# Performance work log

Measured on AMD Instinct MI355X. Metric: run time of the kernel, lower is better.

Reference implementation:

```python
import jax, jax.numpy as jnp
import numpy as np

B, L, D = 4, 4096, 1024
C = 8.0  # fixed exponent scale from the module (self.c = 8)


def setup_inputs() -> dict:
    key = jax.random.key(0)
    ks = jax.random.split(key, 4)
    std = 1.0 / np.sqrt(D)  # kaiming normal, fan_in, linear
    x = jax.random.normal(ks[0], (B, L, D), dtype=jnp.float32)
    Wa = jax.random.normal(ks[1], (D, D), dtype=jnp.float32) * std
    Wx = jax.random.normal(ks[2], (D, D), dtype=jnp.float32) * std
    ba = jnp.zeros((D,), dtype=jnp.float32)
    bx = jnp.zeros((D,), dtype=jnp.float32)
    # lmbd ~ U(0.9, 0.999)
    lmbd = 0.9 + 0.099 * jax.random.uniform(ks[3], (D,), dtype=jnp.float32)
    return {"x": x, "Wa": Wa, "Wx": Wx, "ba": ba, "bx": bx, "lmbd": lmbd}


def reference(x, Wa, Wx, ba, bx, lmbd):
    # a = sigmoid(lmbd) computed once at init in the original module
    log_a = jnp.log(jax.nn.sigmoid(lmbd))  # [D], negative
    # Batched projections upfront (F.linear uses W @ x^T, i.e. x @ W.T)
    r = jax.nn.sigmoid(jnp.einsum('bld,hd->blh', x, Wa) + ba)  # recurrence gate
    i = jax.nn.sigmoid(jnp.einsum('bld,hd->blh', x, Wx) + bx)  # input gate
    a_t = jnp.exp(C * r * log_a)                 # a ** (c * r), [B,L,D]
    b_t = jnp.sqrt(1.0 - a_t * a_t) * (i * x)    # [B,L,D]
    # Linear recurrence h_t = a_t * h_{t-1} + b_t, h_0 = 0
    def step(h, ab):
        at, bt = ab
        h = at * h + bt
        return h, h
    h0 = jnp.zeros((x.shape[0], x.shape[2]), dtype=x.dtype)
    _, y = jax.lax.scan(step, h0, (jnp.swapaxes(a_t, 0, 1), jnp.swapaxes(b_t, 0, 1)))
    return jnp.swapaxes(y, 0, 1)  # [B, L, D]
```

## Files before the change

kernel.cpp:

```cpp
#include <hip/hip_runtime.h>
#include <stdint.h>
#include <math.h>


#define D_DIM 1024
#define L_DIM 4096
#define B_DIM 4
#define M_DIM (B_DIM * L_DIM)
#define N_DIM (2 * D_DIM)
#define K_DIM D_DIM
#define NC 32
#define CL (L_DIM / NC)
#define L2E 1.4426950408889634f

typedef __attribute__((ext_vector_type(8))) short short8;
typedef __attribute__((ext_vector_type(4))) short short4v;
typedef __attribute__((ext_vector_type(4))) float float4v;

__device__ __forceinline__ unsigned short f2bf(float f) {
  unsigned u = __float_as_uint(f);
  u += 0x7fffu + ((u >> 16) & 1u);
  return (unsigned short)(u >> 16);
}
__device__ __forceinline__ float bf2f(unsigned short h) {
  return __uint_as_float((unsigned)h << 16);
}
__device__ __forceinline__ short f2h(float f) {
  _Float16 h = (_Float16)f;
  return __builtin_bit_cast(short, h);
}

#define NX16 (M_DIM * K_DIM / 8)
#define NW16 (N_DIM * K_DIM / 8)

__global__ void pack_all(const float* __restrict__ x, const float* __restrict__ Wa,
                         const float* __restrict__ Wx, short* __restrict__ Xs,
                         short* __restrict__ Ws) {
  int t = blockIdx.x * 256 + threadIdx.x;
  const float* src;
  short8* dst;
  int u;
  if (t < NX16) {
    u = t; src = x; dst = (short8*)Xs;
  } else {
    u = t - NX16;
    if (u >= NW16) return;
    dst = (short8*)Ws;
    int row = ((u >> 11) << 4) | (u & 15);
    src = (row < D_DIM) ? Wa : (Wx - (size_t)D_DIM * K_DIM);
  }
  int r  = u & 15;
  int kc = (u >> 4) & 3;
  int k0 = (u >> 6) & 31;
  int R  = u >> 11;
  int m = R * 16 + r;
  int k = (k0 * 4 + kc) * 8;
  const float4v* s4 = (const float4v*)(src + (size_t)m * 1024 + k);
  float4v v0 = s4[0], v1 = s4[1];
  short8 o;
  o[0] = (short)f2bf(v0.x); o[1] = (short)f2bf(v0.y);
  o[2] = (short)f2bf(v0.z); o[3] = (short)f2bf(v0.w);
  o[4] = (short)f2bf(v1.x); o[5] = (short)f2bf(v1.y);
  o[6] = (short)f2bf(v1.z); o[7] = (short)f2bf(v1.w);
  dst[u] = o;
}

__global__ __launch_bounds__(256, 4) void gemm_gates(
    const short* __restrict__ Xs,
    const short* __restrict__ Ws,
    const float* __restrict__ xf,
    const float* __restrict__ ba,
    const float* __restrict__ bx,
    const float* __restrict__ lmbd,
    short* __restrict__ e_out,
    unsigned short* __restrict__ g_out)
{
  __shared__ __align__(16) char smem[17664];

  const int tile_n = blockIdx.x * 128;
  const int tile_m = blockIdx.y * 128;
  const int tid  = threadIdx.x;
  const int wave = tid >> 6;
  const int lane = tid & 63;
  const int row16 = lane & 15;
  const int quad  = lane >> 4;
  const int wave_m = (wave & 1) * 64;
  const int wave_n = (wave >> 1) * 64;

  short* As = (short*)smem;
  short* Bs = (short*)(smem + 8192);
  char* AsB = smem;
  char* BsB = smem + 8192;

  float4v acc[4][4] = {};

  for (int kk = 0; kk < 32; ++kk) {
#pragma unroll
    for (int p = 0; p < 2; ++p) {
      const int G = p * 4 + wave;
      const size_t RgA = (size_t)((tile_m >> 4) + G);
      const size_t RgB = (size_t)((tile_n >> 4) + G);
      __builtin_amdgcn_global_load_lds(
          (const __attribute__((address_space(1))) void*)(Xs + ((RgA * 32 + kk) * 64 + lane) * 8),
          (__attribute__((address_space(3))) void*)(AsB + G * 1024),
          16, 0, 0);
      __builtin_amdgcn_global_load_lds(
          (const __attribute__((address_space(1))) void*)(Ws + ((RgB * 32 + kk) * 64 + lane) * 8),
          (__attribute__((address_space(3))) void*)(BsB + G * 1024),
          16, 0, 0);
    }
    __syncthreads();

    short8 af[4], bfr[4];
#pragma unroll
    for (int i = 0; i < 4; ++i)
      af[i] = *(const short8*)&As[((wave & 1) * 4 + i) * 512 + lane * 8];
#pragma unroll
    for (int i = 0; i < 4; ++i)
      bfr[i] = *(const short8*)&Bs[((wave >> 1) * 4 + i) * 512 + lane * 8];

#pragma unroll
    for (int mi = 0; mi < 4; ++mi)
#pragma unroll
      for (int ni = 0; ni < 4; ++ni)
        acc[mi][ni] = __builtin_amdgcn_mfma_f32_16x16x32_bf16(af[mi], bfr[ni], acc[mi][ni], 0, 0, 0);
    __syncthreads();
  }

  float* Ts = (float*)smem + (size_t)wave * (16 * 68);
  const int colg = (lane & 15) * 4;
  const int rrow = lane >> 4;
  const bool is_a = (tile_n < D_DIM);
  const int ch0 = (is_a ? tile_n : tile_n - D_DIM) + wave_n + colg;

  float4v bias4, la84;
  if (is_a) {
    bias4 = *(const float4v*)(ba + ch0);
    float4v lm4 = *(const float4v*)(lmbd + ch0);
#pragma unroll
    for (int k = 0; k < 4; ++k)
      la84[k] = -8.0f * __builtin_amdgcn_logf(1.0f + __builtin_amdgcn_exp2f(-lm4[k] * L2E));
  } else {
    bias4 = *(const float4v*)(bx + ch0);
  }

#pragma unroll
  for (int mi = 0; mi < 4; ++mi) {
#pragma unroll
    for (int ni = 0; ni < 4; ++ni)
#pragma unroll
      for (int r = 0; r < 4; ++r)
        Ts[(quad * 4 + r) * 68 + ni * 16 + row16] = acc[mi][ni][r];
#pragma unroll
    for (int j = 0; j < 4; ++j) {
      int lr = j * 4 + rrow;
      float4v z = *(const float4v*)&Ts[lr * 68 + colg];
      size_t gm = (size_t)(tile_m + wave_m + mi * 16 + lr);
      short4v o;
      if (is_a) {
#pragma unroll
        for (int k = 0; k < 4; ++k) {
          float s = __builtin_amdgcn_rcpf(1.0f + __builtin_amdgcn_exp2f(-(z[k] + bias4[k]) * L2E));
          o[k] = f2h(s * la84[k]);
        }
        *(short4v*)(e_out + gm * D_DIM + ch0) = o;
      } else {
        float4v xv = *(const float4v*)(xf + gm * D_DIM + ch0);
#pragma unroll
        for (int k = 0; k < 4; ++k) {
          float s = __builtin_amdgcn_rcpf(1.0f + __builtin_amdgcn_exp2f(-(z[k] + bias4[k]) * L2E));
          o[k] = (short)f2bf(s * xv[k]);
        }
        *(short4v*)((short*)g_out + gm * D_DIM + ch0) = o;
      }
    }
  }
}

__global__ void scan_phase1(const short* __restrict__ e, const unsigned short* __restrict__ g,
                            float* __restrict__ P, float* __restrict__ Q) {
  int d = blockIdx.x * 256 + threadIdx.x;
  int c = blockIdx.y;
  int b = blockIdx.z;
  const size_t base = ((size_t)(b * L_DIM + c * CL)) * D_DIM + d;
  float Pv = 1.0f, Qv = 0.0f;
#pragma unroll 4
  for (int t = 0; t < CL; ++t) {
    float ev = (float)__builtin_bit_cast(_Float16, e[base + (size_t)t * D_DIM]);
    float at = __builtin_amdgcn_exp2f(ev);
    float gv = bf2f(g[base + (size_t)t * D_DIM]);
    float bt = sqrtf(fmaxf(1.0f - at * at, 0.0f)) * gv;
    Qv = fmaf(at, Qv, bt);
    Pv *= at;
  }
  int idx = (b * NC + c) * D_DIM + d;
  P[idx] = Pv;
  Q[idx] = Qv;
}

__global__ void scan_phase3(const short* __restrict__ e, const unsigned short* __restrict__ g,
                            const float* __restrict__ P, const float* __restrict__ Q,
                            float* __restrict__ y) {
  int d = blockIdx.x * 256 + threadIdx.x;
  int c = blockIdx.y;
  int b = blockIdx.z;
  float h = 0.0f;
#pragma unroll 4
  for (int cc = 0; cc < c; ++cc) {
    int idx = (b * NC + cc) * D_DIM + d;
    h = fmaf(P[idx], h, Q[idx]);
  }
  const size_t base = ((size_t)(b * L_DIM + c * CL)) * D_DIM + d;
#pragma unroll 4
  for (int t = 0; t < CL; ++t) {
    float ev = (float)__builtin_bit_cast(_Float16, e[base + (size_t)t * D_DIM]);
    float at = __builtin_amdgcn_exp2f(ev);
    float gv = bf2f(g[base + (size_t)t * D_DIM]);
    float bt = sqrtf(fmaxf(1.0f - at * at, 0.0f)) * gv;
    h = fmaf(at, h, bt);
    y[base + (size_t)t * D_DIM] = h;
  }
}

extern "C" void kernel_launch(void* const* d_in, const int* in_sizes, int n_in,
                              void* d_out, int out_size, void* d_ws, size_t ws_size,
                              hipStream_t stream) {
  const float* x    = (const float*)d_in[0];
  const float* Wa   = (const float*)d_in[1];
  const float* Wx   = (const float*)d_in[2];
  const float* ba   = (const float*)d_in[3];
  const float* bx   = (const float*)d_in[4];
  const float* lmbd = (const float*)d_in[5];
  float* y = (float*)d_out;

  char* ws = (char*)d_ws;
  short* Xs             = (short*)ws;
  short* Wsz            = (short*)(ws + 33554432);
  short* e_buf          = (short*)(ws + 37748736);
  unsigned short* g_buf = (unsigned short*)(ws + 71303168);
  float* P              = (float*)(ws + 104857600);
  float* Q              = (float*)(ws + 105381888);

  pack_all<<<(NX16 + NW16) / 256, 256, 0, stream>>>(x, Wa, Wx, Xs, Wsz);

  dim3 gg(N_DIM / 128, M_DIM / 128);
  gemm_gates<<<gg, 256, 0, stream>>>(Xs, Wsz, x, ba, bx, lmbd, e_buf, g_buf);

  dim3 sg(D_DIM / 256, NC, B_DIM);
  scan_phase1<<<sg, 256, 0, stream>>>(e_buf, g_buf, P, Q);
  scan_phase3<<<sg, 256, 0, stream>>>(e_buf, g_buf, P, Q, y);
}
```

Baseline: 250.5 us.

## Fuse scan phases with decoupled look-back and read bf16 x in gate epilogue

Merges the two scan kernels into one. Each chunk computes its local (P,Q), waits on the previous chunk's published carry through a flag-tagged 64-bit slot, publishes its own carry, then runs the output pass. This removes one kernel launch and the O(NC) serial prefix over P/Q per chunk. The slots are zeroed inside the pack kernel. Separately, the gate epilogue reads x from the packed bf16 buffer instead of fp32, halving that read at a small precision cost. The spin-wait depends on earlier chunks being scheduled first, since the grid is ordered by chunk index, and it serializes the carry chain across 32 chunks.

```diff
diff --git a/kernel.cpp b/kernel.cpp
--- a/kernel.cpp
+++ b/kernel.cpp
@@ -32,22 +32,26 @@
 
 #define NX16 (M_DIM * K_DIM / 8)
 #define NW16 (N_DIM * K_DIM / 8)
+#define NSLOTS (B_DIM * NC * D_DIM)
 
 __global__ void pack_all(const float* __restrict__ x, const float* __restrict__ Wa,
                          const float* __restrict__ Wx, short* __restrict__ Xs,
-                         short* __restrict__ Ws) {
+                         short* __restrict__ Ws, unsigned long long* __restrict__ slots) {
   int t = blockIdx.x * 256 + threadIdx.x;
   const float* src;
   short8* dst;
   int u;
   if (t < NX16) {
     u = t; src = x; dst = (short8*)Xs;
-  } else {
+  } else if (t < NX16 + NW16) {
     u = t - NX16;
-    if (u >= NW16) return;
     dst = (short8*)Ws;
     int row = ((u >> 11) << 4) | (u & 15);
     src = (row < D_DIM) ? Wa : (Wx - (size_t)D_DIM * K_DIM);
+  } else {
+    int s = t - NX16 - NW16;
+    if (s < NSLOTS) slots[s] = 0ULL;
+    return;
   }
   int r  = u & 15;
   int kc = (u >> 4) & 3;
@@ -68,7 +72,6 @@
 __global__ __launch_bounds__(256, 4) void gemm_gates(
     const short* __restrict__ Xs,
     const short* __restrict__ Ws,
-    const float* __restrict__ xf,
     const float* __restrict__ ba,
     const float* __restrict__ bx,
     const float* __restrict__ lmbd,
@@ -143,6 +146,7 @@
   } else {
     bias4 = *(const float4v*)(bx + ch0);
   }
+  const size_t xs_ch = ((size_t)(ch0 >> 5) * 4 + ((ch0 >> 3) & 3)) * 16 * 8 + (ch0 & 7);
 
 #pragma unroll
   for (int mi = 0; mi < 4; ++mi) {
@@ -165,11 +169,11 @@
         }
         *(short4v*)(e_out + gm * D_DIM + ch0) = o;
       } else {
-        float4v xv = *(const float4v*)(xf + gm * D_DIM + ch0);
+        short4v xq = *(const short4v*)(Xs + ((gm >> 4) * 32 * 64 + (gm & 15)) * 8 + xs_ch);
 #pragma unroll
         for (int k = 0; k < 4; ++k) {
           float s = __builtin_amdgcn_rcpf(1.0f + __builtin_amdgcn_exp2f(-(z[k] + bias4[k]) * L2E));
-          o[k] = (short)f2bf(s * xv[k]);
+          o[k] = (short)f2bf(s * bf2f((unsigned short)xq[k]));
         }
         *(short4v*)((short*)g_out + gm * D_DIM + ch0) = o;
       }
@@ -177,12 +181,14 @@
   }
 }
 
-__global__ void scan_phase1(const short* __restrict__ e, const unsigned short* __restrict__ g,
-                            float* __restrict__ P, float* __restrict__ Q) {
+__global__ __launch_bounds__(256) void scan_fused(
+    const short* __restrict__ e, const unsigned short* __restrict__ g,
+    unsigned long long* __restrict__ slots, float* __restrict__ y) {
   int d = blockIdx.x * 256 + threadIdx.x;
   int c = blockIdx.y;
   int b = blockIdx.z;
   const size_t base = ((size_t)(b * L_DIM + c * CL)) * D_DIM + d;
+
   float Pv = 1.0f, Qv = 0.0f;
 #pragma unroll 4
   for (int t = 0; t < CL; ++t) {
@@ -193,24 +199,24 @@
     Qv = fmaf(at, Qv, bt);
     Pv *= at;
   }
-  int idx = (b * NC + c) * D_DIM + d;
-  P[idx] = Pv;
-  Q[idx] = Qv;
-}
-
-__global__ void scan_phase3(const short* __restrict__ e, const unsigned short* __restrict__ g,
-                            const float* __restrict__ P, const float* __restrict__ Q,
-                            float* __restrict__ y) {
-  int d = blockIdx.x * 256 + threadIdx.x;
-  int c = blockIdx.y;
-  int b = blockIdx.z;
-  float h = 0.0f;
-#pragma unroll 4
-  for (int cc = 0; cc < c; ++cc) {
-    int idx = (b * NC + cc) * D_DIM + d;
-    h = fmaf(P[idx], h, Q[idx]);
-  }
-  const size_t base = ((size_t)(b * L_DIM + c * CL)) * D_DIM + d;
+
+  float Hin = 0.0f;
+  if (c > 0) {
+    unsigned long long* sp = slots + ((size_t)(b * NC + c - 1) * D_DIM + d);
+    unsigned long long v = atomicAdd(sp, 0ULL);
+    while ((unsigned)(v >> 32) != 1u) {
+      __builtin_amdgcn_s_sleep(8);
+      v = atomicAdd(sp, 0ULL);
+    }
+    Hin = __uint_as_float((unsigned)v);
+  }
+  if (c < NC - 1) {
+    float Hout = fmaf(Pv, Hin, Qv);
+    atomicExch(slots + ((size_t)(b * NC + c) * D_DIM + d),
+               (1ULL << 32) | (unsigned long long)__float_as_uint(Hout));
+  }
+
+  float h = Hin;
 #pragma unroll 4
   for (int t = 0; t < CL; ++t) {
     float ev = (float)__builtin_bit_cast(_Float16, e[base + (size_t)t * D_DIM]);
@@ -234,19 +240,17 @@
   float* y = (float*)d_out;
 
   char* ws = (char*)d_ws;
-  short* Xs             = (short*)ws;
-  short* Wsz            = (short*)(ws + 33554432);
-  short* e_buf          = (short*)(ws + 37748736);
-  unsigned short* g_buf = (unsigned short*)(ws + 71303168);
-  float* P              = (float*)(ws + 104857600);
-  float* Q              = (float*)(ws + 105381888);
-
-  pack_all<<<(NX16 + NW16) / 256, 256, 0, stream>>>(x, Wa, Wx, Xs, Wsz);
+  short* Xs                  = (short*)ws;
+  short* Wsz                 = (short*)(ws + 33554432);
+  short* e_buf               = (short*)(ws + 37748736);
+  unsigned short* g_buf      = (unsigned short*)(ws + 71303168);
+  unsigned long long* slots  = (unsigned long long*)(ws + 104857600);
+
+  pack_all<<<(NX16 + NW16 + NSLOTS) / 256, 256, 0, stream>>>(x, Wa, Wx, Xs, Wsz, slots);
 
   dim3 gg(N_DIM / 128, M_DIM / 128);
-  gemm_gates<<<gg, 256, 0, stream>>>(Xs, Wsz, x, ba, bx, lmbd, e_buf, g_buf);
+  gemm_gates<<<gg, 256, 0, stream>>>(Xs, Wsz, ba, bx, lmbd, e_buf, g_buf);
 
   dim3 sg(D_DIM / 256, NC, B_DIM);
-  scan_phase1<<<sg, 256, 0, stream>>>(e_buf, g_buf, P, Q);
-  scan_phase3<<<sg, 256, 0, stream>>>(e_buf, g_buf, P, Q, y);
-}
+  scan_fused<<<sg, 256, 0, stream>>>(e_buf, g_buf, slots, y);
+}
```

After: 269.3 us. 7.5% more time.
